# Kernel optimization log

Hardware: AMD Instinct MI355X
Metric: run time of the kernel (lower is better)

The kernel has to match this reference:

```python
import jax, jax.numpy as jnp
import numpy as np

D = 128        # num_hidden
NIN = 384      # num_in (edge feature dim)
FF = 4 * D     # dense inner dim
SCALE = 30.0
EPS = 1e-5     # haiku LayerNorm default

gelu = lambda x: jax.nn.gelu(x, approximate=False)

def _ln(x, g, o):
    mu = jnp.mean(x, axis=-1, keepdims=True)
    var = jnp.var(x, axis=-1, keepdims=True)
    return (x - mu) * jax.lax.rsqrt(var + EPS) * g + o

def setup_inputs() -> dict:
    key = jax.random.key(0)
    ks = jax.random.split(key, 12)
    B, N, K = 4, 2048, 48
    s = lambda fan_in: 1.0 / np.sqrt(fan_in)
    return {
        "h_V": jax.random.normal(ks[0], (B, N, D), jnp.float32),
        "h_E": jax.random.normal(ks[1], (B, N, K, NIN), jnp.float32),
        "mask_V": jnp.ones((B, N), jnp.float32),
        "mask_attend": jnp.ones((B, N, K), jnp.float32),
        "W1": jax.random.normal(ks[2], (D + NIN, D), jnp.float32) * s(D + NIN),
        "b1": jnp.zeros((D,), jnp.float32),
        "W2": jax.random.normal(ks[3], (D, D), jnp.float32) * s(D),
        "b2": jnp.zeros((D,), jnp.float32),
        "W3": jax.random.normal(ks[4], (D, D), jnp.float32) * s(D),
        "b3": jnp.zeros((D,), jnp.float32),
        "W_in": jax.random.normal(ks[5], (D, FF), jnp.float32) * s(D),
        "b_in": jnp.zeros((FF,), jnp.float32),
        "W_out": jax.random.normal(ks[6], (FF, D), jnp.float32) * s(FF),
        "b_out": jnp.zeros((D,), jnp.float32),
        "g1": jnp.ones((D,), jnp.float32),
        "o1": jnp.zeros((D,), jnp.float32),
        "g2": jnp.ones((D,), jnp.float32),
        "o2": jnp.zeros((D,), jnp.float32),
    }

def reference(h_V, h_E, mask_V, mask_attend, W1, b1, W2, b2, W3, b3,
              W_in, b_in, W_out, b_out, g1, o1, g2, o2):
    B, N, K, _ = h_E.shape
    # broadcast node feats over neighbors and concat with edge feats: (B,N,K,D+NIN)
    h_V_exp = jnp.broadcast_to(h_V[:, :, None, :], (B, N, K, h_V.shape[-1]))
    h_EV = jnp.concatenate([h_V_exp, h_E], axis=-1)
    h = gelu(h_EV @ W1 + b1)
    h = gelu(h @ W2 + b2)
    h_message = h @ W3 + b3                      # (B,N,K,D)
    h_message = mask_attend[..., None] * h_message
    dh = jnp.sum(h_message, axis=-2) / SCALE      # (B,N,D)
    h_V = _ln(h_V + dh, g1, o1)                   # dropout rate=0 -> identity
    dh = gelu(h_V @ W_in + b_in) @ W_out + b_out  # position-wise FFN
    h_V = _ln(h_V + dh, g2, o2)
    h_V = mask_V[..., None] * h_V
    return h_V
```

## Files before the change

kernel.cpp:

```cpp
#include <hip/hip_runtime.h>
#include <hip/hip_bf16.h>

typedef unsigned short u16;
typedef __attribute__((ext_vector_type(8))) short short8;
typedef __attribute__((ext_vector_type(4))) float f32x4;

#define SD   128
#define SNIN 384
#define SK   48
#define FPAD 520

#define OFF_W1A   0
#define OFF_W1B   32768
#define OFF_W2    131072
#define OFF_W3    163840
#define OFF_WIN   196608
#define OFF_WOUT  327680

__device__ __forceinline__ u16 f2b(float f){
  union { float f; unsigned u; } v; v.f = f;
  unsigned r = (v.u + 0x7FFFu + ((v.u >> 16) & 1u)) >> 16;
  return (u16)r;
}
__device__ __forceinline__ short8 ldg8(const u16* p){
  return *reinterpret_cast<const short8*>(p);
}
__device__ __forceinline__ short8 pack8(float4 a, float4 b){
  union { unsigned u[4]; short8 s; } r;
  asm("v_cvt_pk_bf16_f32 %0, %1, %2" : "=v"(r.u[0]) : "v"(a.x), "v"(a.y));
  asm("v_cvt_pk_bf16_f32 %0, %1, %2" : "=v"(r.u[1]) : "v"(a.z), "v"(a.w));
  asm("v_cvt_pk_bf16_f32 %0, %1, %2" : "=v"(r.u[2]) : "v"(b.x), "v"(b.y));
  asm("v_cvt_pk_bf16_f32 %0, %1, %2" : "=v"(r.u[3]) : "v"(b.z), "v"(b.w));
  return r.s;
}
__device__ __forceinline__ short8 cvt8(const float* p){
  float4 a = *reinterpret_cast<const float4*>(p);
  float4 b = *reinterpret_cast<const float4*>(p + 4);
  return pack8(a, b);
}
__device__ __forceinline__ void gl_lds16(const float* g, float* l){
  __builtin_amdgcn_global_load_lds((const __attribute__((address_space(1))) void*)g,
                                   (__attribute__((address_space(3))) void*)l, 16, 0, 0);
}

__device__ __forceinline__ float gelu_f(float x){
  float xc = fminf(3.0f, fmaxf(-3.0f, x));
  float u  = xc*xc;
  float p  = fmaf(u, fmaf(u, fmaf(u, -4.81034e-4f, 1.185750e-2f), -1.1877797e-1f), 7.9165011e-1f);
  float t  = xc*p;
  float hx = 0.5f*x;
  return fmaf(t, hx, hx);
}

__global__ __launch_bounds__(256) void prep_pack(
    const float* __restrict__ W1, const float* __restrict__ W2, const float* __restrict__ W3,
    const float* __restrict__ Win, const float* __restrict__ Wout, u16* __restrict__ ws)
{
  int t = blockIdx.x*256 + threadIdx.x;
  const float* src; int stride, rowoff, NT; u16* dst; int local;
  if (t < 2048)       { src=W1;  stride=SD;  rowoff=0;   NT=8;  dst=ws+OFF_W1A/2;  local=t;       }
  else if (t < 8192)  { src=W1;  stride=SD;  rowoff=128; NT=8;  dst=ws+OFF_W1B/2;  local=t-2048;  }
  else if (t < 10240) { src=W2;  stride=SD;  rowoff=0;   NT=8;  dst=ws+OFF_W2/2;   local=t-8192;  }
  else if (t < 12288) { src=W3;  stride=SD;  rowoff=0;   NT=8;  dst=ws+OFF_W3/2;   local=t-10240; }
  else if (t < 20480) { src=Win; stride=512; rowoff=0;   NT=32; dst=ws+OFF_WIN/2;  local=t-12288; }
  else                { src=Wout;stride=SD;  rowoff=0;   NT=8;  dst=ws+OFF_WOUT/2; local=t-20480; }
  int lane = local & 63;
  int blk  = local >> 6;
  int nt = blk % NT, ks = blk / NT;
  int k0 = rowoff + ks*32 + (lane>>4)*8;
  int n  = nt*16 + (lane & 15);
  union { u16 a[8]; short8 v; } tmp;
  #pragma unroll
  for (int j=0;j<8;j++) tmp.a[j] = f2b(src[(size_t)(k0+j)*stride + n]);
  *reinterpret_cast<short8*>(dst + (size_t)local*8) = tmp.v;
}

__global__ __launch_bounds__(256, 4) void dec_nodes(
    const float* __restrict__ hV, const float* __restrict__ hE, const float* __restrict__ mAtt,
    const float* __restrict__ b1, const float* __restrict__ b2, const float* __restrict__ b3,
    const float* __restrict__ g1, const float* __restrict__ o1,
    const u16* __restrict__ ws, float* __restrict__ u_out)
{
  __shared__ __align__(16) float STG[2][1536];
  __shared__ __align__(16) u16   HHs[48*128];
  __shared__ float LNS[8];

  const int tid  = threadIdx.x;
  const int w    = tid >> 6;
  const int lane = tid & 63;
  const int quad = lane >> 4;
  const int l16  = lane & 15;
  const int g    = blockIdx.x;
  const int n0   = w*2;

  const float* gsrcl = hE + (size_t)g*(SK*SNIN) + (size_t)(lane>>3)*SNIN
                          + (size_t)(((lane&7) ^ (lane>>3))*4);

  #define STAGE(ks, buf) { \
    if (w < 2){ gl_lds16(gsrcl + (size_t)(2*w)*8*SNIN   + (ks)*32, &STG[buf][(2*w)*256]);   \
                gl_lds16(gsrcl + (size_t)(2*w+1)*8*SNIN + (ks)*32, &STG[buf][(2*w+1)*256]); } \
    else      { gl_lds16(gsrcl + (size_t)(w+2)*8*SNIN   + (ks)*32, &STG[buf][(w+2)*256]);   } }

  STAGE(0, 0);

  float base1v[2];
  {
    f32x4 accb[2] = {(f32x4){0.f,0.f,0.f,0.f},(f32x4){0.f,0.f,0.f,0.f}};
    const float* hp = hV + (size_t)g*SD + quad*8;
    const u16* Bb1 = ws + OFF_W1A/2 + (size_t)lane*8;
    #pragma unroll
    for (int ks=0; ks<4; ks++){
      short8 af = cvt8(hp + ks*32);
      #pragma unroll
      for (int j=0;j<2;j++){
        short8 bf = ldg8(Bb1 + ((size_t)(ks*8 + n0 + j)*64)*8);
        accb[j] = __builtin_amdgcn_mfma_f32_16x16x32_bf16(af, bf, accb[j], 0,0,0);
      }
    }
    #pragma unroll
    for (int j=0;j<2;j++) base1v[j] = accb[j][0] + b1[(n0+j)*16 + l16];
  }

  const u16* BbG1 = ws + OFF_W1B/2 + (size_t)lane*8;
  short8 bq0 = ldg8(BbG1 + ((size_t)(n0)*64)*8);
  short8 bq1 = ldg8(BbG1 + ((size_t)(n0+1)*64)*8);
  __syncthreads();

  f32x4 acc[3][2];
  #pragma unroll
  for (int mt=0;mt<3;mt++){ acc[mt][0]=(f32x4){0.f,0.f,0.f,0.f}; acc[mt][1]=(f32x4){0.f,0.f,0.f,0.f}; }

  #pragma unroll
  for (int ks=0; ks<12; ks++){
    short8 bn0, bn1;
    if (ks < 11){
      bn0 = ldg8(BbG1 + ((size_t)((ks+1)*8 + n0)*64)*8);
      bn1 = ldg8(BbG1 + ((size_t)((ks+1)*8 + n0+1)*64)*8);
      STAGE(ks+1, (ks+1)&1);
    }
    const float* bufF = STG[ks&1];
    short8 af[3];
    #pragma unroll
    for (int mt=0;mt<3;mt++){
      int row = mt*16 + l16;
      int sp0 = (2*quad) ^ (l16 & 7);
      float4 a = *reinterpret_cast<const float4*>(bufF + row*32 + sp0*4);
      float4 b = *reinterpret_cast<const float4*>(bufF + row*32 + (sp0^1)*4);
      af[mt] = pack8(a, b);
    }
    #pragma unroll
    for (int mt=0;mt<3;mt++){
      acc[mt][0] = __builtin_amdgcn_mfma_f32_16x16x32_bf16(af[mt], bq0, acc[mt][0], 0,0,0);
      acc[mt][1] = __builtin_amdgcn_mfma_f32_16x16x32_bf16(af[mt], bq1, acc[mt][1], 0,0,0);
    }
    __syncthreads();
    if (ks < 11){ bq0 = bn0; bq1 = bn1; }
  }

  #pragma unroll
  for (int mt=0; mt<3; mt++)
    #pragma unroll
    for (int j=0; j<2; j++)
      #pragma unroll
      for (int i=0;i<4;i++){
        int row = mt*16 + quad*4 + i;
        int col = (n0+j)*16 + l16;
        HHs[row*128 + (((col>>3) ^ (row&15))<<3) + (col&7)] = f2b(gelu_f(acc[mt][j][i] + base1v[j]));
      }
  __syncthreads();

  #pragma unroll
  for (int mt=0;mt<3;mt++){ acc[mt][0]=(f32x4){0.f,0.f,0.f,0.f}; acc[mt][1]=(f32x4){0.f,0.f,0.f,0.f}; }
  {
    const u16* Bb = ws + OFF_W2/2 + (size_t)lane*8;
    #pragma unroll
    for (int ks=0; ks<4; ks++){
      short8 afm[3];
      #pragma unroll
      for (int mt=0; mt<3; mt++){
        int row = mt*16 + l16;
        int sp  = (ks*4 + quad) ^ l16;
        afm[mt] = *reinterpret_cast<const short8*>(HHs + row*128 + sp*8);
      }
      #pragma unroll
      for (int j=0;j<2;j++){
        short8 bf = ldg8(Bb + ((size_t)(ks*8 + n0 + j)*64)*8);
        #pragma unroll
        for (int mt=0;mt<3;mt++)
          acc[mt][j] = __builtin_amdgcn_mfma_f32_16x16x32_bf16(afm[mt], bf, acc[mt][j], 0,0,0);
      }
    }
  }
  __syncthreads();
  #pragma unroll
  for (int mt=0; mt<3; mt++)
    #pragma unroll
    for (int j=0; j<2; j++){
      float bb = b2[(n0+j)*16 + l16];
      #pragma unroll
      for (int i=0;i<4;i++){
        int row = mt*16 + quad*4 + i;
        int col = (n0+j)*16 + l16;
        HHs[row*128 + (((col>>3) ^ (row&15))<<3) + (col&7)] = f2b(gelu_f(acc[mt][j][i] + bb));
      }
    }
  __syncthreads();

  #pragma unroll
  for (int mt=0;mt<3;mt++){ acc[mt][0]=(f32x4){0.f,0.f,0.f,0.f}; acc[mt][1]=(f32x4){0.f,0.f,0.f,0.f}; }
  {
    const u16* Bb = ws + OFF_W3/2 + (size_t)lane*8;
    #pragma unroll
    for (int ks=0; ks<4; ks++){
      short8 afm[3];
      #pragma unroll
      for (int mt=0; mt<3; mt++){
        int row = mt*16 + l16;
        int sp  = (ks*4 + quad) ^ l16;
        afm[mt] = *reinterpret_cast<const short8*>(HHs + row*128 + sp*8);
      }
      #pragma unroll
      for (int j=0;j<2;j++){
        short8 bf = ldg8(Bb + ((size_t)(ks*8 + n0 + j)*64)*8);
        #pragma unroll
        for (int mt=0;mt<3;mt++)
          acc[mt][j] = __builtin_amdgcn_mfma_f32_16x16x32_bf16(afm[mt], bf, acc[mt][j], 0,0,0);
      }
    }
  }
  float p0 = 0.f, p1 = 0.f;
  {
    float b3v0 = b3[(n0)*16 + l16], b3v1 = b3[(n0+1)*16 + l16];
    #pragma unroll
    for (int mt=0; mt<3; mt++)
      #pragma unroll
      for (int i=0;i<4;i++){
        float m = mAtt[(size_t)g*SK + mt*16 + quad*4 + i];
        p0 = fmaf(m, acc[mt][0][i] + b3v0, p0);
        p1 = fmaf(m, acc[mt][1][i] + b3v1, p1);
      }
    p0 += __shfl_down(p0, 32, 64); p0 += __shfl_down(p0, 16, 64); p0 = __shfl(p0, l16, 64);
    p1 += __shfl_down(p1, 32, 64); p1 += __shfl_down(p1, 16, 64); p1 = __shfl(p1, l16, 64);
  }

  {
    float x0 = hV[(size_t)g*SD + (n0)*16   + l16] + p0*(1.0f/30.0f);
    float x1 = hV[(size_t)g*SD + (n0+1)*16 + l16] + p1*(1.0f/30.0f);
    float s = x0 + x1;
    float q = fmaf(x0, x0, x1*x1);
    #pragma unroll
    for (int off=1; off<64; off<<=1){ s += __shfl_xor(s, off, 64); q += __shfl_xor(q, off, 64); }
    if (lane == 0){ LNS[w] = s; LNS[4+w] = q; }
    __syncthreads();
    s = LNS[0]+LNS[1]+LNS[2]+LNS[3];
    q = LNS[4]+LNS[5]+LNS[6]+LNS[7];
    float mu  = s * (1.0f/512.0f);
    float var = q * (1.0f/512.0f) - mu*mu;
    float rs  = rsqrtf(var + 1e-5f);
    if (quad == 0){
      int c0 = (n0)*16 + l16, c1 = (n0+1)*16 + l16;
      u_out[(size_t)g*SD + c0] = (x0-mu)*rs*g1[c0] + o1[c0];
      u_out[(size_t)g*SD + c1] = (x1-mu)*rs*g1[c1] + o1[c1];
    }
  }
  #undef STAGE
}

__global__ __launch_bounds__(256) void ffn_ln(
    const float* __restrict__ b_in, const float* __restrict__ b_out,
    const float* __restrict__ g2, const float* __restrict__ o2, const float* __restrict__ mV,
    const u16* __restrict__ ws, float* __restrict__ uo)
{
  __shared__ u16 fS[16*FPAD];
  __shared__ float dS[16][132];
  const int tid = threadIdx.x, w = tid>>6, lane = tid&63, quad = lane>>4, l16 = lane&15;
  const int m0 = blockIdx.x*16;

  short8 afr[4];
  const float* Ap = uo + (size_t)(m0 + l16)*SD + quad*8;
  #pragma unroll
  for (int ks=0; ks<4; ks++) afr[ks] = cvt8(Ap + ks*32);

  {
    f32x4 acc[8];
    #pragma unroll
    for (int t=0;t<8;t++) acc[t] = (f32x4){0.f,0.f,0.f,0.f};
    const u16* Bp = ws + OFF_WIN/2 + ((size_t)(w*8)*64 + lane)*8;
    #pragma unroll
    for (int ks=0; ks<4; ks++){
      #pragma unroll
      for (int t=0;t<8;t++){
        short8 bf = ldg8(Bp + ((size_t)ks*32 + t)*512);
        acc[t] = __builtin_amdgcn_mfma_f32_16x16x32_bf16(afr[ks], bf, acc[t], 0,0,0);
      }
    }
    #pragma unroll
    for (int t=0;t<8;t++){
      int coln = w*128 + t*16 + l16;
      float bi = b_in[coln];
      #pragma unroll
      for (int i=0;i<4;i++)
        fS[(quad*4+i)*FPAD + coln] = f2b(gelu_f(acc[t][i] + bi));
    }
  }
  __syncthreads();

  {
    f32x4 acc2[2];
    acc2[0] = (f32x4){0.f,0.f,0.f,0.f};
    acc2[1] = (f32x4){0.f,0.f,0.f,0.f};
    const u16* Bo = ws + OFF_WOUT/2 + (size_t)lane*8;
    #pragma unroll
    for (int ks=0; ks<16; ks++){
      const short8 af = *reinterpret_cast<const short8*>(&fS[l16*FPAD + ks*32 + quad*8]);
      #pragma unroll
      for (int j=0;j<2;j++){
        short8 bf = ldg8(Bo + ((size_t)ks*8 + (w*2+j))*512);
        acc2[j] = __builtin_amdgcn_mfma_f32_16x16x32_bf16(af, bf, acc2[j], 0,0,0);
      }
    }
    #pragma unroll
    for (int j=0;j<2;j++){
      int cl = (w*2+j)*16 + l16;
      float bo = b_out[cl];
      #pragma unroll
      for (int i=0;i<4;i++)
        dS[quad*4+i][cl] = acc2[j][i] + bo;
    }
  }
  __syncthreads();

  {
    int rl = w*4 + quad;
    int r  = m0 + rl;
    float xv[8]; float s = 0.f, q = 0.f;
    #pragma unroll
    for (int t=0;t<8;t++){
      xv[t] = uo[(size_t)r*SD + t*16 + l16] + dS[rl][t*16 + l16];
      s += xv[t]; q = fmaf(xv[t], xv[t], q);
    }
    #pragma unroll
    for (int mk=1; mk<16; mk<<=1){ s += __shfl_xor(s, mk, 64); q += __shfl_xor(q, mk, 64); }
    float mu  = s * (1.0f/128.0f);
    float var = q * (1.0f/128.0f) - mu*mu;
    float rs  = rsqrtf(var + 1e-5f);
    float mv  = mV[r];
    #pragma unroll
    for (int t=0;t<8;t++){
      int cl = t*16 + l16;
      uo[(size_t)r*SD + cl] = mv * ((xv[t]-mu)*rs*g2[cl] + o2[cl]);
    }
  }
}

extern "C" void kernel_launch(void* const* d_in, const int* in_sizes, int n_in,
                              void* d_out, int out_size, void* d_ws, size_t ws_size,
                              hipStream_t stream) {
  (void)n_in; (void)out_size; (void)ws_size;
  const float* hV    = (const float*)d_in[0];
  const float* hE    = (const float*)d_in[1];
  const float* mV    = (const float*)d_in[2];
  const float* mAtt  = (const float*)d_in[3];
  const float* W1    = (const float*)d_in[4];
  const float* b1    = (const float*)d_in[5];
  const float* W2    = (const float*)d_in[6];
  const float* b2    = (const float*)d_in[7];
  const float* W3    = (const float*)d_in[8];
  const float* b3    = (const float*)d_in[9];
  const float* Win   = (const float*)d_in[10];
  const float* b_in  = (const float*)d_in[11];
  const float* Wout  = (const float*)d_in[12];
  const float* b_out = (const float*)d_in[13];
  const float* g1    = (const float*)d_in[14];
  const float* o1    = (const float*)d_in[15];
  const float* g2    = (const float*)d_in[16];
  const float* o2    = (const float*)d_in[17];
  u16*   ws   = (u16*)d_ws;
  float* outp = (float*)d_out;
  const int NG = in_sizes[0] / SD;

  hipLaunchKernelGGL(prep_pack, dim3(112), dim3(256), 0, stream, W1, W2, W3, Win, Wout, ws);
  hipLaunchKernelGGL(dec_nodes, dim3(NG), dim3(256), 0, stream,
                     hV, hE, mAtt, b1, b2, b3, g1, o1, ws, outp);
  hipLaunchKernelGGL(ffn_ln, dim3(NG/16), dim3(256), 0, stream,
                     b_in, b_out, g2, o2, mV, ws, outp);
}
```

Measured before the change: 862.5 us.

## Load whole edge tile to LDS as bf16 upfront instead of double-buffered staging

```diff
diff --git a/kernel.cpp b/kernel.cpp
--- a/kernel.cpp
+++ b/kernel.cpp
@@ -37,10 +37,6 @@
   float4 a = *reinterpret_cast<const float4*>(p);
   float4 b = *reinterpret_cast<const float4*>(p + 4);
   return pack8(a, b);
-}
-__device__ __forceinline__ void gl_lds16(const float* g, float* l){
-  __builtin_amdgcn_global_load_lds((const __attribute__((address_space(1))) void*)g,
-                                   (__attribute__((address_space(3))) void*)l, 16, 0, 0);
 }
 
 __device__ __forceinline__ float gelu_f(float x){
@@ -81,8 +77,7 @@
     const float* __restrict__ g1, const float* __restrict__ o1,
     const u16* __restrict__ ws, float* __restrict__ u_out)
 {
-  __shared__ __align__(16) float STG[2][1536];
-  __shared__ __align__(16) u16   HHs[48*128];
+  __shared__ __align__(16) u16 HEs[48*384];
   __shared__ float LNS[8];
 
   const int tid  = threadIdx.x;
@@ -93,15 +88,22 @@
   const int g    = blockIdx.x;
   const int n0   = w*2;
 
-  const float* gsrcl = hE + (size_t)g*(SK*SNIN) + (size_t)(lane>>3)*SNIN
-                          + (size_t)(((lane&7) ^ (lane>>3))*4);
-
-  #define STAGE(ks, buf) { \
-    if (w < 2){ gl_lds16(gsrcl + (size_t)(2*w)*8*SNIN   + (ks)*32, &STG[buf][(2*w)*256]);   \
-                gl_lds16(gsrcl + (size_t)(2*w+1)*8*SNIN + (ks)*32, &STG[buf][(2*w+1)*256]); } \
-    else      { gl_lds16(gsrcl + (size_t)(w+2)*8*SNIN   + (ks)*32, &STG[buf][(w+2)*256]);   } }
-
-  STAGE(0, 0);
+  const float* hEn = hE + (size_t)g*(SK*SNIN);
+  #define SLD3(s0, RA, RB) { _Pragma("unroll") for (int q=0;q<3;q++){ int G=((s0)+q)*256+tid; \
+      RA[q] = *reinterpret_cast<const float4*>(hEn + (size_t)G*8); \
+      RB[q] = *reinterpret_cast<const float4*>(hEn + (size_t)G*8 + 4); } }
+  #define SWR3(s0, RA, RB) { _Pragma("unroll") for (int q=0;q<3;q++){ int G=((s0)+q)*256+tid; \
+      int r = G/48, c = G - r*48; \
+      *reinterpret_cast<short8*>(HEs + r*384 + ((c ^ (r&7))<<3)) = pack8(RA[q], RB[q]); } }
+  {
+    float4 ra[3], rb[3], rc[3], rd[3];
+    SLD3(0, ra, rb);
+    SLD3(3, rc, rd);
+    SWR3(0, ra, rb);
+    SLD3(6, ra, rb);
+    SWR3(3, rc, rd);
+    SWR3(6, ra, rb);
+  }
 
   float base1v[2];
   {
@@ -120,42 +122,34 @@
     #pragma unroll
     for (int j=0;j<2;j++) base1v[j] = accb[j][0] + b1[(n0+j)*16 + l16];
   }
-
-  const u16* BbG1 = ws + OFF_W1B/2 + (size_t)lane*8;
-  short8 bq0 = ldg8(BbG1 + ((size_t)(n0)*64)*8);
-  short8 bq1 = ldg8(BbG1 + ((size_t)(n0+1)*64)*8);
   __syncthreads();
 
   f32x4 acc[3][2];
   #pragma unroll
   for (int mt=0;mt<3;mt++){ acc[mt][0]=(f32x4){0.f,0.f,0.f,0.f}; acc[mt][1]=(f32x4){0.f,0.f,0.f,0.f}; }
-
-  #pragma unroll
-  for (int ks=0; ks<12; ks++){
-    short8 bn0, bn1;
-    if (ks < 11){
-      bn0 = ldg8(BbG1 + ((size_t)((ks+1)*8 + n0)*64)*8);
-      bn1 = ldg8(BbG1 + ((size_t)((ks+1)*8 + n0+1)*64)*8);
-      STAGE(ks+1, (ks+1)&1);
-    }
-    const float* bufF = STG[ks&1];
-    short8 af[3];
-    #pragma unroll
-    for (int mt=0;mt<3;mt++){
-      int row = mt*16 + l16;
-      int sp0 = (2*quad) ^ (l16 & 7);
-      float4 a = *reinterpret_cast<const float4*>(bufF + row*32 + sp0*4);
-      float4 b = *reinterpret_cast<const float4*>(bufF + row*32 + (sp0^1)*4);
-      af[mt] = pack8(a, b);
-    }
-    #pragma unroll
-    for (int mt=0;mt<3;mt++){
-      acc[mt][0] = __builtin_amdgcn_mfma_f32_16x16x32_bf16(af[mt], bq0, acc[mt][0], 0,0,0);
-      acc[mt][1] = __builtin_amdgcn_mfma_f32_16x16x32_bf16(af[mt], bq1, acc[mt][1], 0,0,0);
-    }
-    __syncthreads();
-    if (ks < 11){ bq0 = bn0; bq1 = bn1; }
-  }
+  {
+    const u16* BbG1 = ws + OFF_W1B/2 + (size_t)lane*8;
+    short8 bq0 = ldg8(BbG1 + ((size_t)(n0)*64)*8);
+    short8 bq1 = ldg8(BbG1 + ((size_t)(n0+1)*64)*8);
+    #pragma unroll
+    for (int ks=0; ks<12; ks++){
+      short8 bn0, bn1;
+      if (ks < 11){
+        bn0 = ldg8(BbG1 + ((size_t)((ks+1)*8 + n0)*64)*8);
+        bn1 = ldg8(BbG1 + ((size_t)((ks+1)*8 + n0+1)*64)*8);
+      }
+      #pragma unroll
+      for (int mt=0;mt<3;mt++){
+        int row = mt*16 + l16;
+        short8 af = *reinterpret_cast<const short8*>(
+                      HEs + row*384 + (((ks*4 + quad) ^ (row&7))<<3));
+        acc[mt][0] = __builtin_amdgcn_mfma_f32_16x16x32_bf16(af, bq0, acc[mt][0], 0,0,0);
+        acc[mt][1] = __builtin_amdgcn_mfma_f32_16x16x32_bf16(af, bq1, acc[mt][1], 0,0,0);
+      }
+      if (ks < 11){ bq0 = bn0; bq1 = bn1; }
+    }
+  }
+  __syncthreads();
 
   #pragma unroll
   for (int mt=0; mt<3; mt++)
@@ -165,7 +159,7 @@
       for (int i=0;i<4;i++){
         int row = mt*16 + quad*4 + i;
         int col = (n0+j)*16 + l16;
-        HHs[row*128 + (((col>>3) ^ (row&15))<<3) + (col&7)] = f2b(gelu_f(acc[mt][j][i] + base1v[j]));
+        HEs[row*128 + (((col>>3) ^ (row&15))<<3) + (col&7)] = f2b(gelu_f(acc[mt][j][i] + base1v[j]));
       }
   __syncthreads();
 
@@ -180,7 +174,7 @@
       for (int mt=0; mt<3; mt++){
         int row = mt*16 + l16;
         int sp  = (ks*4 + quad) ^ l16;
-        afm[mt] = *reinterpret_cast<const short8*>(HHs + row*128 + sp*8);
+        afm[mt] = *reinterpret_cast<const short8*>(HEs + row*128 + sp*8);
       }
       #pragma unroll
       for (int j=0;j<2;j++){
@@ -201,7 +195,7 @@
       for (int i=0;i<4;i++){
         int row = mt*16 + quad*4 + i;
         int col = (n0+j)*16 + l16;
-        HHs[row*128 + (((col>>3) ^ (row&15))<<3) + (col&7)] = f2b(gelu_f(acc[mt][j][i] + bb));
+        HEs[row*128 + (((col>>3) ^ (row&15))<<3) + (col&7)] = f2b(gelu_f(acc[mt][j][i] + bb));
       }
     }
   __syncthreads();
@@ -217,7 +211,7 @@
       for (int mt=0; mt<3; mt++){
         int row = mt*16 + l16;
         int sp  = (ks*4 + quad) ^ l16;
-        afm[mt] = *reinterpret_cast<const short8*>(HHs + row*128 + sp*8);
+        afm[mt] = *reinterpret_cast<const short8*>(HEs + row*128 + sp*8);
       }
       #pragma unroll
       for (int j=0;j<2;j++){
@@ -263,7 +257,8 @@
       u_out[(size_t)g*SD + c1] = (x1-mu)*rs*g1[c1] + o1[c1];
     }
   }
-  #undef STAGE
+  #undef SLD3
+  #undef SWR3
 }
 
 __global__ __launch_bounds__(256) void ffn_ln(
```

New measurement: 849.4 us. About the same (-1.5%).
